# Kernel tuning notes

Hardware: AMD Instinct MI355X
Metric: run time of the kernel (lower is better)

## Reference

```python
import jax, jax.numpy as jnp
import numpy as np

V, H, T = 32000, 768, 32
TYPES, MAX_VISITS, SEGS = 9, 512, 3
B, S = 32, 2048
EPS = 1e-12


def setup_inputs() -> dict:
    key = jax.random.key(0)
    ks = jax.random.split(key, 16)
    input_ids = jax.random.randint(ks[0], (B, S), 0, V)
    type_ids = jax.random.randint(ks[1], (B, S), 0, TYPES)
    time_stamps = jax.random.uniform(ks[2], (B, S), dtype=jnp.float32)
    ages = jax.random.uniform(ks[3], (B, S), dtype=jnp.float32)
    visit_orders = jax.random.randint(ks[4], (B, S), 0, MAX_VISITS)
    visit_segments = jax.random.randint(ks[5], (B, S), 0, SEGS)
    # parameters
    W_word = jax.random.normal(ks[6], (V, H), jnp.float32) * 0.02
    W_word = W_word.at[0].set(0.0)  # padding_idx = 0
    W_type = jax.random.normal(ks[7], (TYPES, H), jnp.float32) * 0.02
    W_order = jax.random.normal(ks[8], (MAX_VISITS, H), jnp.float32) * 0.02
    W_seg = jax.random.normal(ks[9], (SEGS, H), jnp.float32) * 0.02
    time_w = jax.random.normal(ks[10], (1, T), jnp.float32)
    time_phi = jax.random.normal(ks[11], (1, T), jnp.float32)
    age_w = jax.random.normal(ks[12], (1, T), jnp.float32)
    age_phi = jax.random.normal(ks[13], (1, T), jnp.float32)
    lin_W = jax.random.normal(ks[14], (H + 2 * T, H), jnp.float32) * 0.02
    lin_b = jnp.zeros((H,), jnp.float32)
    ln_g = jnp.ones((H,), jnp.float32)
    ln_beta = jnp.zeros((H,), jnp.float32)
    return dict(input_ids=input_ids, type_ids=type_ids, time_stamps=time_stamps,
                ages=ages, visit_orders=visit_orders, visit_segments=visit_segments,
                W_word=W_word, W_type=W_type, W_order=W_order, W_seg=W_seg,
                time_w=time_w, time_phi=time_phi, age_w=age_w, age_phi=age_phi,
                lin_W=lin_W, lin_b=lin_b, ln_g=ln_g, ln_beta=ln_beta)


def _sinusoidal(t, w, phi):
    # t: [B,S]; w,phi: [1,T] -> [B,S,T]
    return jnp.sin(t[..., None] * w + phi)


def reference(input_ids, type_ids, time_stamps, ages, visit_orders, visit_segments,
              W_word, W_type, W_order, W_seg, time_w, time_phi, age_w, age_phi,
              lin_W, lin_b, ln_g, ln_beta):
    word = W_word[input_ids]                       # [B,S,H]
    # time delta embedding (is_time_delta=True)
    dt = jnp.concatenate([time_stamps[:, :1] * 0.0,
                          time_stamps[:, 1:] - time_stamps[:, :-1]], axis=-1)
    time_e = _sinusoidal(dt, time_w, time_phi)     # [B,S,T]
    age_e = _sinusoidal(ages, age_w, age_phi)      # [B,S,T]
    seg_e = W_seg[visit_segments]                  # [B,S,H]
    order_e = W_order[visit_orders]                # [B,S,H]
    type_e = W_type[type_ids]                      # [B,S,H]
    fused = jnp.concatenate([word, time_e, age_e], axis=-1)   # [B,S,H+2T]
    fused = jnp.tanh(fused @ lin_W + lin_b)        # [B,S,H]
    emb = fused + type_e + order_e + seg_e
    # dropout is identity in eval mode; LayerNorm(eps=1e-12)
    mu = jnp.mean(emb, axis=-1, keepdims=True)
    var = jnp.mean(jnp.square(emb - mu), axis=-1, keepdims=True)
    return (emb - mu) * jax.lax.rsqrt(var + EPS) * ln_g + ln_beta
```

## Files before the change

### kernel.cpp

```cpp
#include <hip/hip_runtime.h>
#include <hip/hip_bf16.h>
#include <math.h>
#include <stdint.h>

#define HH 768
#define TT 32
#define KK 832
#define SS 2048
#define NSTEP 26

typedef __attribute__((ext_vector_type(4))) float f32x4;
typedef __attribute__((ext_vector_type(8))) short bf16x8;
typedef __attribute__((ext_vector_type(4))) short bf16x4;

__device__ __forceinline__ short f2bf(float f) {
  union { float f; uint32_t u; } v; v.f = f;
  uint32_t u = v.u;
  return (short)((u + 0x7FFFu + ((u >> 16) & 1u)) >> 16);
}

__global__ void transpose_w_kernel(const float* __restrict__ lin_W,
                                   short* __restrict__ bt) {
  int i = blockIdx.x * 256 + threadIdx.x;
  if (i >= HH * KK) return;
  int n = i / KK;
  int k = i - n * KK;
  bt[i] = f2bf(lin_W[(size_t)k * HH + n]);
}

template <bool WS>
__global__ __launch_bounds__(512, 1) void ehr_kernel(
    const int* __restrict__ input_ids, const int* __restrict__ type_ids,
    const float* __restrict__ time_stamps, const float* __restrict__ ages,
    const int* __restrict__ visit_orders, const int* __restrict__ visit_segments,
    const float* __restrict__ W_word, const float* __restrict__ W_type,
    const float* __restrict__ W_order, const float* __restrict__ W_seg,
    const float* __restrict__ time_w, const float* __restrict__ time_phi,
    const float* __restrict__ age_w, const float* __restrict__ age_phi,
    const float* __restrict__ lin_W, const float* __restrict__ lin_b,
    const float* __restrict__ ln_g, const float* __restrict__ ln_beta,
    const short* __restrict__ bt_ws, float* __restrict__ out) {
  __shared__ short Bt[HH * 32];
  __shared__ short Atile[64 * 32];
  __shared__ float dtl[64], agel[64];
  __shared__ int idl[64], tyl[64], orl[64], sgl[64];
  __shared__ float tpar[128];
  __shared__ float redS[4][64], redQ[4][64];

  const int tid = threadIdx.x;
  const int t0 = blockIdx.x * 64;

  if (tid < 128) {
    int j = tid & 31;
    float v;
    if (tid < 32) v = time_w[j];
    else if (tid < 64) v = time_phi[j];
    else if (tid < 96) v = age_w[j];
    else v = age_phi[j];
    tpar[tid] = v;
  }
  if (tid < 64) {
    int t = t0 + tid;
    int s = t & (SS - 1);
    float tsv = time_stamps[t];
    dtl[tid] = (s == 0) ? 0.f : (tsv - time_stamps[t - 1]);
    agel[tid] = ages[t];
    idl[tid] = input_ids[t];
    tyl[tid] = type_ids[t];
    orl[tid] = visit_orders[t];
    sgl[tid] = visit_segments[t];
  }
  __syncthreads();

  const int lane = tid & 63, wave = tid >> 6;
  const int wm = wave >> 2, wn = wave & 3;
  const int l15 = lane & 15, l4 = lane >> 4;

  const int arow = tid >> 3, ac = tid & 7;
  const int myid = idl[arow];
  const float mydt = dtl[arow];
  const float myage = agel[arow];
  const float* wrow = W_word + (size_t)myid * HH;

  f32x4 acc[2][12];
#pragma unroll
  for (int mf = 0; mf < 2; ++mf)
#pragma unroll
    for (int nf = 0; nf < 12; ++nf) acc[mf][nf] = (f32x4)(0.0f);

  for (int st = 0; st < NSTEP; ++st) {
    const int k0 = st * 32;
    {
      int kg = k0 + ac * 4;
      bf16x4 w4;
      if (kg < HH) {
        const f32x4 v = *(const f32x4*)(wrow + kg);
        w4[0] = f2bf(v[0]); w4[1] = f2bf(v[1]);
        w4[2] = f2bf(v[2]); w4[3] = f2bf(v[3]);
      } else {
        int isAge = (kg >= HH + TT);
        int j = kg - (isAge ? (HH + TT) : HH);
        float x = isAge ? myage : mydt;
        int wof = isAge ? 64 : 0;
#pragma unroll
        for (int i = 0; i < 4; ++i)
          w4[i] = f2bf(sinf(x * tpar[wof + j + i] + tpar[wof + 32 + j + i]));
      }
      *(bf16x4*)(Atile + tid * 4) = w4;
    }
    if (WS) {
#pragma unroll
      for (int p = 0; p < 6; ++p) {
        int chunk = p * 8 + wave;
        short* ldst = Bt + chunk * 512;
        int n = chunk * 16 + (lane >> 2);
        int q = lane & 3;
        const short* src = bt_ws + (size_t)n * KK + k0 + q * 8;
        __builtin_amdgcn_global_load_lds(
            (const __attribute__((address_space(1))) unsigned int*)src,
            (__attribute__((address_space(3))) unsigned int*)ldst, 16, 0, 0);
      }
    } else {
#pragma unroll
      for (int i6 = 0; i6 < 6; ++i6) {
        int c = i6 * 512 + tid;
        int n = c >> 2, q = c & 3;
        int kb = k0 + q * 8;
        bf16x8 w8;
#pragma unroll
        for (int j = 0; j < 8; ++j) w8[j] = f2bf(lin_W[(size_t)(kb + j) * HH + n]);
        *(bf16x8*)(Bt + n * 32 + q * 8) = w8;
      }
    }
    __syncthreads();

    const bf16x8* Af = (const bf16x8*)Atile;
    const bf16x8* Bf = (const bf16x8*)Bt;
    bf16x8 a0 = Af[(wm * 32 + l15) * 4 + l4];
    bf16x8 a1 = Af[(wm * 32 + 16 + l15) * 4 + l4];
#pragma unroll
    for (int nf = 0; nf < 12; ++nf) {
      int n = wn * 192 + nf * 16 + l15;
      bf16x8 b = Bf[n * 4 + l4];
      acc[0][nf] = __builtin_amdgcn_mfma_f32_16x16x32_bf16(a0, b, acc[0][nf], 0, 0, 0);
      acc[1][nf] = __builtin_amdgcn_mfma_f32_16x16x32_bf16(a1, b, acc[1][nf], 0, 0, 0);
    }
    __syncthreads();
  }

  float sp[2][4], sq[2][4];
#pragma unroll
  for (int mf = 0; mf < 2; ++mf)
#pragma unroll
    for (int r = 0; r < 4; ++r) { sp[mf][r] = 0.f; sq[mf][r] = 0.f; }

#pragma unroll
  for (int nf = 0; nf < 12; ++nf) {
    int n = wn * 192 + nf * 16 + l15;
    float bias = lin_b[n];
#pragma unroll
    for (int mf = 0; mf < 2; ++mf) {
#pragma unroll
      for (int r = 0; r < 4; ++r) {
        int row = wm * 32 + mf * 16 + l4 * 4 + r;
        float z = tanhf(acc[mf][nf][r] + bias);
        z += W_type[(size_t)tyl[row] * HH + n];
        z += W_order[(size_t)orl[row] * HH + n];
        z += W_seg[(size_t)sgl[row] * HH + n];
        acc[mf][nf][r] = z;
        sp[mf][r] += z;
        sq[mf][r] += z * z;
      }
    }
  }
#pragma unroll
  for (int m = 1; m < 16; m <<= 1) {
#pragma unroll
    for (int mf = 0; mf < 2; ++mf)
#pragma unroll
      for (int r = 0; r < 4; ++r) {
        sp[mf][r] += __shfl_xor(sp[mf][r], m, 64);
        sq[mf][r] += __shfl_xor(sq[mf][r], m, 64);
      }
  }
  if (l15 == 0) {
#pragma unroll
    for (int mf = 0; mf < 2; ++mf)
#pragma unroll
      for (int r = 0; r < 4; ++r) {
        int row = wm * 32 + mf * 16 + l4 * 4 + r;
        redS[wn][row] = sp[mf][r];
        redQ[wn][row] = sq[mf][r];
      }
  }
  __syncthreads();

  float mu[2][4], rs[2][4];
#pragma unroll
  for (int mf = 0; mf < 2; ++mf)
#pragma unroll
    for (int r = 0; r < 4; ++r) {
      int row = wm * 32 + mf * 16 + l4 * 4 + r;
      float s = redS[0][row] + redS[1][row] + redS[2][row] + redS[3][row];
      float q = redQ[0][row] + redQ[1][row] + redQ[2][row] + redQ[3][row];
      float m_ = s * (1.0f / 768.0f);
      float v_ = q * (1.0f / 768.0f) - m_ * m_;
      if (v_ < 0.f) v_ = 0.f;
      mu[mf][r] = m_;
      rs[mf][r] = rsqrtf(v_ + 1e-12f);
    }

#pragma unroll
  for (int nf = 0; nf < 12; ++nf) {
    int n = wn * 192 + nf * 16 + l15;
    float g = ln_g[n], be = ln_beta[n];
#pragma unroll
    for (int mf = 0; mf < 2; ++mf) {
#pragma unroll
      for (int r = 0; r < 4; ++r) {
        int row = wm * 32 + mf * 16 + l4 * 4 + r;
        out[(size_t)(t0 + row) * HH + n] =
            (acc[mf][nf][r] - mu[mf][r]) * rs[mf][r] * g + be;
      }
    }
  }
}

extern "C" void kernel_launch(void* const* d_in, const int* in_sizes, int n_in,
                              void* d_out, int out_size, void* d_ws, size_t ws_size,
                              hipStream_t stream) {
  const int* input_ids = (const int*)d_in[0];
  const int* type_ids = (const int*)d_in[1];
  const float* time_stamps = (const float*)d_in[2];
  const float* ages = (const float*)d_in[3];
  const int* visit_orders = (const int*)d_in[4];
  const int* visit_segments = (const int*)d_in[5];
  const float* W_word = (const float*)d_in[6];
  const float* W_type = (const float*)d_in[7];
  const float* W_order = (const float*)d_in[8];
  const float* W_seg = (const float*)d_in[9];
  const float* time_w = (const float*)d_in[10];
  const float* time_phi = (const float*)d_in[11];
  const float* age_w = (const float*)d_in[12];
  const float* age_phi = (const float*)d_in[13];
  const float* lin_W = (const float*)d_in[14];
  const float* lin_b = (const float*)d_in[15];
  const float* ln_g = (const float*)d_in[16];
  const float* ln_beta = (const float*)d_in[17];
  float* out = (float*)d_out;

  const size_t bt_bytes = (size_t)HH * KK * sizeof(short);
  const bool use_ws = (d_ws != nullptr) && (ws_size >= bt_bytes);

  if (use_ws) {
    short* bt = (short*)d_ws;
    transpose_w_kernel<<<dim3((HH * KK + 255) / 256), dim3(256), 0, stream>>>(lin_W, bt);
    ehr_kernel<true><<<dim3(1024), dim3(512), 0, stream>>>(
        input_ids, type_ids, time_stamps, ages, visit_orders, visit_segments,
        W_word, W_type, W_order, W_seg, time_w, time_phi, age_w, age_phi,
        lin_W, lin_b, ln_g, ln_beta, (const short*)bt, out);
  } else {
    ehr_kernel<false><<<dim3(1024), dim3(512), 0, stream>>>(
        input_ids, type_ids, time_stamps, ages, visit_orders, visit_segments,
        W_word, W_type, W_order, W_seg, time_w, time_phi, age_w, age_phi,
        lin_W, lin_b, ln_g, ln_beta, nullptr, out);
  }
}
```

Measured before the change: 574.6 us.

## Split gather into separate bf16 A-matrix kernel and use direct-to-LDS loads in GEMM

Adds a pre-pass kernel that gathers word embeddings and computes the sinusoidal time/age features for every token, writing a bf16 A matrix into the workspace. The GEMM kernel then streams A and B tiles with global_load_lds straight into shared memory, with no per-step gather or conversion. The aim is to pull the irregular gather and transcendental work out of the MFMA loop. In exchange it adds an extra round trip through HBM for a roughly 109 MB bf16 intermediate, plus one more kernel launch, and it needs a larger workspace or the old path is used.

```diff
diff --git a/kernel.cpp b/kernel.cpp
--- a/kernel.cpp
+++ b/kernel.cpp
@@ -8,6 +8,7 @@
 #define KK 832
 #define SS 2048
 #define NSTEP 26
+#define NTOK 65536
 
 typedef __attribute__((ext_vector_type(4))) float f32x4;
 typedef __attribute__((ext_vector_type(8))) short bf16x8;
@@ -28,8 +29,202 @@
   bt[i] = f2bf(lin_W[(size_t)k * HH + n]);
 }
 
+__global__ __launch_bounds__(256) void gather_a_kernel(
+    const int* __restrict__ input_ids, const float* __restrict__ ts,
+    const float* __restrict__ ages, const float* __restrict__ W_word,
+    const float* __restrict__ time_w, const float* __restrict__ time_phi,
+    const float* __restrict__ age_w, const float* __restrict__ age_phi,
+    short* __restrict__ Aws) {
+  const int wave = threadIdx.x >> 6, lane = threadIdx.x & 63;
+  const int t = blockIdx.x * 4 + wave;
+  if (t >= NTOK) return;
+  const float* wrow = W_word + (size_t)input_ids[t] * HH;
+  const int s = t & (SS - 1);
+  const float dt = (s == 0) ? 0.f : (ts[t] - ts[t - 1]);
+  const float age = ages[t];
+  short* dst = Aws + (size_t)t * KK;
+#pragma unroll
+  for (int c2 = 0; c2 < 2; ++c2) {
+    int chunk = c2 * 64 + lane;
+    if (chunk < 104) {
+      int k = chunk * 8;
+      bf16x8 v;
+      if (k < HH) {
+        f32x4 x0 = *(const f32x4*)(wrow + k);
+        f32x4 x1 = *(const f32x4*)(wrow + k + 4);
+        v[0] = f2bf(x0[0]); v[1] = f2bf(x0[1]); v[2] = f2bf(x0[2]); v[3] = f2bf(x0[3]);
+        v[4] = f2bf(x1[0]); v[5] = f2bf(x1[1]); v[6] = f2bf(x1[2]); v[7] = f2bf(x1[3]);
+      } else if (k < HH + TT) {
+        int j = k - HH;
+#pragma unroll
+        for (int i = 0; i < 8; ++i)
+          v[i] = f2bf(sinf(dt * time_w[j + i] + time_phi[j + i]));
+      } else {
+        int j = k - HH - TT;
+#pragma unroll
+        for (int i = 0; i < 8; ++i)
+          v[i] = f2bf(sinf(age * age_w[j + i] + age_phi[j + i]));
+      }
+      *(bf16x8*)(dst + k) = v;
+    }
+  }
+}
+
+__global__ __launch_bounds__(512, 1) void ehr_gemm_kernel(
+    const int* __restrict__ type_ids, const int* __restrict__ visit_orders,
+    const int* __restrict__ visit_segments, const float* __restrict__ W_type,
+    const float* __restrict__ W_order, const float* __restrict__ W_seg,
+    const float* __restrict__ lin_b, const float* __restrict__ ln_g,
+    const float* __restrict__ ln_beta, const short* __restrict__ Aws,
+    const short* __restrict__ Btw, float* __restrict__ out) {
+  __shared__ short Bt[HH * 32];
+  __shared__ short Atile[64 * 32];
+  __shared__ int tyl[64], orl[64], sgl[64];
+  __shared__ float redS[4][64], redQ[4][64];
+
+  const int tid = threadIdx.x;
+  const int t0 = blockIdx.x * 64;
+  if (tid < 64) {
+    tyl[tid] = type_ids[t0 + tid];
+    orl[tid] = visit_orders[t0 + tid];
+    sgl[tid] = visit_segments[t0 + tid];
+  }
+  const int lane = tid & 63, wave = tid >> 6;
+  const int wm = wave >> 2, wn = wave & 3;
+  const int l15 = lane & 15, l4 = lane >> 4;
+
+  f32x4 acc[2][12];
+#pragma unroll
+  for (int mf = 0; mf < 2; ++mf)
+#pragma unroll
+    for (int nf = 0; nf < 12; ++nf) acc[mf][nf] = (f32x4)(0.0f);
+
+  const size_t a_lane_off = (size_t)l15 * KK + l4 * 8;
+
+  for (int st = 0; st < NSTEP; ++st) {
+    const int k0 = st * 32;
+    if (wave < 4) {
+      const short* src = Aws + (size_t)(t0 + wave * 16) * KK + a_lane_off + k0;
+      __builtin_amdgcn_global_load_lds(
+          (const __attribute__((address_space(1))) unsigned int*)src,
+          (__attribute__((address_space(3))) unsigned int*)(Atile + wave * 512),
+          16, 0, 0);
+    }
+#pragma unroll
+    for (int p = 0; p < 6; ++p) {
+      int c = p * 8 + wave;
+      const short* src = Btw + (size_t)(c * 16) * KK + a_lane_off + k0;
+      __builtin_amdgcn_global_load_lds(
+          (const __attribute__((address_space(1))) unsigned int*)src,
+          (__attribute__((address_space(3))) unsigned int*)(Bt + c * 512),
+          16, 0, 0);
+    }
+    __syncthreads();
+
+    const bf16x8* Af = (const bf16x8*)Atile;
+    const bf16x8* Bf = (const bf16x8*)Bt;
+    bf16x8 a0 = Af[(wm * 2 + 0) * 64 + l4 * 16 + l15];
+    bf16x8 a1 = Af[(wm * 2 + 1) * 64 + l4 * 16 + l15];
+#pragma unroll
+    for (int nf = 0; nf < 12; ++nf) {
+      bf16x8 b = Bf[(wn * 12 + nf) * 64 + l4 * 16 + l15];
+      acc[0][nf] = __builtin_amdgcn_mfma_f32_16x16x32_bf16(a0, b, acc[0][nf], 0, 0, 0);
+      acc[1][nf] = __builtin_amdgcn_mfma_f32_16x16x32_bf16(a1, b, acc[1][nf], 0, 0, 0);
+    }
+    __syncthreads();
+  }
+
+  float sp[2][4], sq[2][4];
+#pragma unroll
+  for (int mf = 0; mf < 2; ++mf)
+#pragma unroll
+    for (int r = 0; r < 4; ++r) { sp[mf][r] = 0.f; sq[mf][r] = 0.f; }
+
+#pragma unroll
+  for (int nf = 0; nf < 12; ++nf) {
+    int n = wn * 192 + nf * 16 + l15;
+    float bias = lin_b[n];
+#pragma unroll
+    for (int mf = 0; mf < 2; ++mf) {
+#pragma unroll
+      for (int r = 0; r < 4; ++r) {
+        int row = wm * 32 + mf * 16 + l4 * 4 + r;
+        float z = tanhf(acc[mf][nf][r] + bias);
+        z += W_type[(size_t)tyl[row] * HH + n];
+        z += W_order[(size_t)orl[row] * HH + n];
+        z += W_seg[(size_t)sgl[row] * HH + n];
+        acc[mf][nf][r] = z;
+        sp[mf][r] += z;
+        sq[mf][r] += z * z;
+      }
+    }
+  }
+#pragma unroll
+  for (int m = 1; m < 16; m <<= 1) {
+#pragma unroll
+    for (int mf = 0; mf < 2; ++mf)
+#pragma unroll
+      for (int r = 0; r < 4; ++r) {
+        sp[mf][r] += __shfl_xor(sp[mf][r], m, 64);
+        sq[mf][r] += __shfl_xor(sq[mf][r], m, 64);
+      }
+  }
+  if (l15 == 0) {
+#pragma unroll
+    for (int mf = 0; mf < 2; ++mf)
+#pragma unroll
+      for (int r = 0; r < 4; ++r) {
+        int row = wm * 32 + mf * 16 + l4 * 4 + r;
+        redS[wn][row] = sp[mf][r];
+        redQ[wn][row] = sq[mf][r];
+      }
+  }
+  __syncthreads();
+
+  float mu[2][4], rs[2][4];
+#pragma unroll
+  for (int mf = 0; mf < 2; ++mf)
+#pragma unroll
+    for (int r = 0; r < 4; ++r) {
+      int row = wm * 32 + mf * 16 + l4 * 4 + r;
+      float s = redS[0][row] + redS[1][row] + redS[2][row] + redS[3][row];
+      float q = redQ[0][row] + redQ[1][row] + redQ[2][row] + redQ[3][row];
+      float m_ = s * (1.0f / 768.0f);
+      float v_ = q * (1.0f / 768.0f) - m_ * m_;
+      if (v_ < 0.f) v_ = 0.f;
+      mu[mf][r] = m_;
+      rs[mf][r] = rsqrtf(v_ + 1e-12f);
+    }
+
+  float* Os = (float*)Bt;
+#pragma unroll 1
+  for (int g = 0; g < 4; ++g) {
+    int gw = g >> 1, gm = g & 1;
+    __syncthreads();
+    if (wm == gw) {
+#pragma unroll
+      for (int nf = 0; nf < 12; ++nf) {
+        int n = wn * 192 + nf * 16 + l15;
+        float gg = ln_g[n], be = ln_beta[n];
+#pragma unroll
+        for (int r = 0; r < 4; ++r) {
+          int lr = l4 * 4 + r;
+          Os[lr * HH + n] = (acc[gm][nf][r] - mu[gm][r]) * rs[gm][r] * gg + be;
+        }
+      }
+    }
+    __syncthreads();
+    float* ob = out + (size_t)(t0 + g * 16) * HH;
+#pragma unroll
+    for (int q = 0; q < 6; ++q) {
+      int idx4 = q * 512 + tid;
+      ((f32x4*)ob)[idx4] = ((const f32x4*)Os)[idx4];
+    }
+  }
+}
+
 template <bool WS>
-__global__ __launch_bounds__(512, 1) void ehr_kernel(
+__global__ __launch_bounds__(512, 1) void ehr_fallback(
     const int* __restrict__ input_ids, const int* __restrict__ type_ids,
     const float* __restrict__ time_stamps, const float* __restrict__ ages,
     const int* __restrict__ visit_orders, const int* __restrict__ visit_segments,
@@ -75,7 +270,6 @@
   const int lane = tid & 63, wave = tid >> 6;
   const int wm = wave >> 2, wn = wave & 3;
   const int l15 = lane & 15, l4 = lane >> 4;
-
   const int arow = tid >> 3, ac = tid & 7;
   const int myid = idl[arow];
   const float mydt = dtl[arow];
@@ -249,18 +443,27 @@
   const float* ln_beta = (const float*)d_in[17];
   float* out = (float*)d_out;
 
+  const size_t a_bytes = (size_t)NTOK * KK * sizeof(short);
   const size_t bt_bytes = (size_t)HH * KK * sizeof(short);
-  const bool use_ws = (d_ws != nullptr) && (ws_size >= bt_bytes);
-
-  if (use_ws) {
+
+  if (d_ws != nullptr && ws_size >= a_bytes + bt_bytes) {
+    short* Aws = (short*)d_ws;
+    short* Btw = (short*)((char*)d_ws + a_bytes);
+    transpose_w_kernel<<<dim3((HH * KK + 255) / 256), dim3(256), 0, stream>>>(lin_W, Btw);
+    gather_a_kernel<<<dim3(NTOK / 4), dim3(256), 0, stream>>>(
+        input_ids, time_stamps, ages, W_word, time_w, time_phi, age_w, age_phi, Aws);
+    ehr_gemm_kernel<<<dim3(NTOK / 64), dim3(512), 0, stream>>>(
+        type_ids, visit_orders, visit_segments, W_type, W_order, W_seg,
+        lin_b, ln_g, ln_beta, (const short*)Aws, (const short*)Btw, out);
+  } else if (d_ws != nullptr && ws_size >= bt_bytes) {
     short* bt = (short*)d_ws;
     transpose_w_kernel<<<dim3((HH * KK + 255) / 256), dim3(256), 0, stream>>>(lin_W, bt);
-    ehr_kernel<true><<<dim3(1024), dim3(512), 0, stream>>>(
+    ehr_fallback<true><<<dim3(1024), dim3(512), 0, stream>>>(
         input_ids, type_ids, time_stamps, ages, visit_orders, visit_segments,
         W_word, W_type, W_order, W_seg, time_w, time_phi, age_w, age_phi,
         lin_W, lin_b, ln_g, ln_beta, (const short*)bt, out);
   } else {
-    ehr_kernel<false><<<dim3(1024), dim3(512), 0, stream>>>(
+    ehr_fallback<false><<<dim3(1024), dim3(512), 0, stream>>>(
         input_ids, type_ids, time_stamps, ages, visit_orders, visit_segments,
         W_word, W_type, W_order, W_seg, time_w, time_phi, age_w, age_phi,
         lin_W, lin_b, ln_g, ln_beta, nullptr, out);
```

Measured after the change: 1.169 ms. 103% more time.
